# Optimization experiments

Hardware: AMD Instinct MI355X
Metric: run time of the kernel (lower is better)

The kernel has to match this reference:

```python
import jax, jax.numpy as jnp
import numpy as np

B, N_ITEMS, H1, H2 = 1024, 50000, 600, 200


def setup_inputs() -> dict:
    key = jax.random.key(0)
    ks = jax.random.split(key, 8)
    return {
        "x": jax.random.uniform(ks[0], (B, N_ITEMS), dtype=jnp.float32),
        "W1": jax.random.normal(ks[1], (N_ITEMS, H1), dtype=jnp.float32) * 0.02,
        "b1": jax.random.normal(ks[2], (H1,), dtype=jnp.float32) * 0.001,
        "W2": jax.random.normal(ks[3], (H1, H2), dtype=jnp.float32) * 0.05,
        "b2": jax.random.normal(ks[4], (H2,), dtype=jnp.float32) * 0.001,
        "W3": jax.random.normal(ks[5], (H2, H1), dtype=jnp.float32) * 0.05,
        "b3": jax.random.normal(ks[6], (H1,), dtype=jnp.float32) * 0.001,
        "item_emb": jax.random.normal(ks[7], (N_ITEMS, H1), dtype=jnp.float32) * 0.02,
    }


def reference(x, W1, b1, W2, b2, W3, b3, item_emb):
    # F.normalize(input): L2-normalize rows with eps clamp
    norm = jnp.sqrt(jnp.sum(x * x, axis=-1, keepdims=True))
    h = x / jnp.maximum(norm, 1e-12)
    # tanh MLP stack (dropout is identity at inference)
    h = jnp.tanh(h @ W1 + b1)   # [B, 600]
    h = jnp.tanh(h @ W2 + b2)   # [B, 200]
    h = jnp.tanh(h @ W3 + b3)   # [B, 600]
    # pairwise squared-L2 distance to all item embeddings via GEMM decomposition:
    # ||h||^2 - 2 h.e + ||e||^2  (same math as the broadcasted (h-e)^2 sum)
    h_sq = jnp.sum(h * h, axis=-1, keepdims=True)          # [B, 1]
    e_sq = jnp.sum(item_emb * item_emb, axis=-1)           # [N]
    dist = h_sq - 2.0 * (h @ item_emb.T) + e_sq            # [B, N]
    return dist
```

## Files before the change

kernel.cpp:

```cpp
#include <hip/hip_runtime.h>
#include <stdint.h>

namespace {

constexpr int BROWS = 1024;
constexpr int NIT   = 50000;
constexpr int NH1   = 600;
constexpr int NH2   = 200;
constexpr int KXP   = 50048;
constexpr int N1P   = 640;
constexpr int NEP   = 50048;
constexpr int KEP   = 608;
constexpr int KI_TOTAL = KXP / 32;

typedef _Float16 f16x8 __attribute__((ext_vector_type(8)));
typedef _Float16 f16x4 __attribute__((ext_vector_type(4)));
typedef _Float16 f16x2 __attribute__((ext_vector_type(2)));
typedef float    f32x4 __attribute__((ext_vector_type(4)));

__device__ __forceinline__ void gld16(const void* g, void* l) {
  __builtin_amdgcn_global_load_lds(
      (__attribute__((address_space(1))) void*)(void*)g,
      (__attribute__((address_space(3))) void*)l, 16, 0, 0);
}

__global__ __launch_bounds__(256) void norm_conv_k(const float* __restrict__ x,
                                                   float* __restrict__ invnorm,
                                                   _Float16* __restrict__ xh) {
  const int row = blockIdx.x;
  const float4* xr = (const float4*)(x + (size_t)row * NIT);
  float ss = 0.f;
  if (xh != nullptr) {
    f16x4* xo = (f16x4*)(xh + (size_t)row * KXP);
    #pragma unroll 4
    for (int i = threadIdx.x; i < NIT / 4; i += 256) {
      float4 v = xr[i];
      ss += v.x * v.x + v.y * v.y + v.z * v.z + v.w * v.w;
      f16x4 h;
      h.x = (_Float16)v.x; h.y = (_Float16)v.y;
      h.z = (_Float16)v.z; h.w = (_Float16)v.w;
      xo[i] = h;
    }
    if (threadIdx.x < (KXP - NIT) / 4) {
      f16x4 z;
      z.x = (_Float16)0.f; z.y = (_Float16)0.f;
      z.z = (_Float16)0.f; z.w = (_Float16)0.f;
      xo[NIT / 4 + threadIdx.x] = z;
    }
  } else {
    #pragma unroll 4
    for (int i = threadIdx.x; i < NIT / 4; i += 256) {
      float4 v = xr[i];
      ss += v.x * v.x + v.y * v.y + v.z * v.z + v.w * v.w;
    }
  }
  for (int o = 32; o > 0; o >>= 1) ss += __shfl_down(ss, o);
  __shared__ float red[4];
  if ((threadIdx.x & 63) == 0) red[threadIdx.x >> 6] = ss;
  __syncthreads();
  if (threadIdx.x == 0) {
    float s = red[0] + red[1] + red[2] + red[3];
    invnorm[row] = 1.0f / fmaxf(sqrtf(s), 1e-12f);
  }
}

__global__ __launch_bounds__(256) void transpose_w1_k(const float* __restrict__ W1,
                                                      _Float16* __restrict__ W1T) {
  __shared__ float tile[64][65];
  const int kb = blockIdx.x * 64;
  const int nb = blockIdx.y * 64;
  const int t = threadIdx.x;
  #pragma unroll
  for (int i = 0; i < 16; ++i) {
    int idx = i * 256 + t;
    int k = idx >> 6, n = idx & 63;
    int gk = kb + k, gn = nb + n;
    tile[k][n] = (gk < NIT && gn < NH1) ? W1[(size_t)gk * NH1 + gn] : 0.f;
  }
  __syncthreads();
  #pragma unroll
  for (int i = 0; i < 8; ++i) {
    int idx = i * 256 + t;
    int n = idx >> 5;
    int k2 = (idx & 31) * 2;
    f16x2 h;
    h.x = (_Float16)tile[k2][n];
    h.y = (_Float16)tile[k2 + 1][n];
    *(f16x2*)(&W1T[(size_t)(nb + n) * KXP + kb + k2]) = h;
  }
}

__global__ __launch_bounds__(256) void prep_emb_k(const float* __restrict__ emb,
                                                  _Float16* __restrict__ embb,
                                                  float* __restrict__ esq) {
  const int row = blockIdx.x * 4 + (threadIdx.x >> 6);
  const int lane = threadIdx.x & 63;
  const float* er = emb + (size_t)row * NH1;
  float ss = 0.f;
  #pragma unroll
  for (int j = 0; j < 10; ++j) {
    int idx = lane + 64 * j;
    float v = (row < NIT && idx < NH1) ? er[idx] : 0.f;
    ss += v * v;
    if (idx < KEP) embb[(size_t)row * KEP + idx] = (_Float16)v;
  }
  for (int o = 32; o > 0; o >>= 1) ss += __shfl_down(ss, o);
  if (lane == 0) esq[row] = ss;
}

template <int MODE>
__global__ __launch_bounds__(256, 4) void mfma_nt_k(
    const void* __restrict__ Av, const _Float16* __restrict__ Bg,
    float* __restrict__ Cout, const float* __restrict__ hsq,
    const float* __restrict__ esq) {
  __shared__ _Float16 As[2][128 * 32];
  __shared__ _Float16 Bs[2][128 * 32];

  const int t = threadIdx.x;
  const int n0 = blockIdx.x * 128;
  const int m0 = blockIdx.y * 128;

  int ki0, ki1, lda, ldb;
  if (MODE == 1) {
    ki0 = 0; ki1 = KEP / 32; lda = KEP; ldb = KEP;
  } else {
    const int Z = (int)gridDim.z;
    const int kiPer = (KI_TOTAL + Z - 1) / Z;
    ki0 = blockIdx.z * kiPer;
    ki1 = ki0 + kiPer;
    if (ki1 > KI_TOTAL) ki1 = KI_TOTAL;
    lda = (MODE == 0) ? NIT : KXP;
    ldb = KXP;
  }

  const int lane = t & 63;
  const int wid = t >> 6;
  const int wm = wid >> 1, wn = wid & 1;
  const int lrow = lane & 15, quad = lane >> 4;

  const f32x4 zero = {0.f, 0.f, 0.f, 0.f};
  f32x4 acc[4][4];
  #pragma unroll
  for (int i = 0; i < 4; ++i)
    #pragma unroll
    for (int j = 0; j < 4; ++j) acc[i][j] = zero;

  auto stage = [&](int buf, int ki) {
    const int k0 = ki * 32;
    if (MODE == 0) {
      const float* A = (const float*)Av;
      #pragma unroll
      for (int j = 0; j < 4; ++j) {
        int g = j * 256 + t;
        int row = g >> 3;
        int kq = (g & 7) * 4;
        float4 v = {0.f, 0.f, 0.f, 0.f};
        if (k0 + kq < NIT)
          v = *(const float4*)(A + (size_t)(m0 + row) * lda + (k0 + kq));
        f16x4 h;
        h.x = (_Float16)v.x; h.y = (_Float16)v.y;
        h.z = (_Float16)v.z; h.w = (_Float16)v.w;
        *(f16x4*)(&As[buf][row * 32 + kq]) = h;
      }
    } else {
      const _Float16* A = (const _Float16*)Av;
      #pragma unroll
      for (int j = 0; j < 2; ++j) {
        int c = j * 256 + t;
        int row = c >> 2, kk = (c & 3) * 8;
        gld16(A + (size_t)(m0 + row) * lda + (k0 + kk), &As[buf][c * 8]);
      }
    }
    #pragma unroll
    for (int j = 0; j < 2; ++j) {
      int c = j * 256 + t;
      int row = c >> 2, kk = (c & 3) * 8;
      gld16(Bg + (size_t)(n0 + row) * ldb + (k0 + kk), &Bs[buf][c * 8]);
    }
  };

  stage(0, ki0);
  __syncthreads();

  int cur = 0;
  for (int ki = ki0; ki < ki1; ++ki) {
    if (ki + 1 < ki1) stage(cur ^ 1, ki + 1);

    f16x8 af[4], bfr[4];
    #pragma unroll
    for (int mi = 0; mi < 4; ++mi)
      af[mi] = *(const f16x8*)(&As[cur][(wm * 64 + mi * 16 + lrow) * 32 + quad * 8]);
    #pragma unroll
    for (int ni = 0; ni < 4; ++ni)
      bfr[ni] = *(const f16x8*)(&Bs[cur][(wn * 64 + ni * 16 + lrow) * 32 + quad * 8]);
    #pragma unroll
    for (int mi = 0; mi < 4; ++mi)
      #pragma unroll
      for (int ni = 0; ni < 4; ++ni)
        acc[mi][ni] = __builtin_amdgcn_mfma_f32_16x16x32_f16(af[mi], bfr[ni],
                                                             acc[mi][ni], 0, 0, 0);
    __syncthreads();
    cur ^= 1;
  }

  if (MODE != 1) {
    float* Cs = Cout + (size_t)blockIdx.z * BROWS * N1P;
    #pragma unroll
    for (int mi = 0; mi < 4; ++mi)
      #pragma unroll
      for (int r = 0; r < 4; ++r) {
        int row = m0 + wm * 64 + mi * 16 + quad * 4 + r;
        #pragma unroll
        for (int ni = 0; ni < 4; ++ni) {
          int col = n0 + wn * 64 + ni * 16 + lrow;
          Cs[(size_t)row * N1P + col] = acc[mi][ni][r];
        }
      }
  } else {
    #pragma unroll
    for (int mi = 0; mi < 4; ++mi)
      #pragma unroll
      for (int r = 0; r < 4; ++r) {
        int row = m0 + wm * 64 + mi * 16 + quad * 4 + r;
        float hv = hsq[row];
        #pragma unroll
        for (int ni = 0; ni < 4; ++ni) {
          int col = n0 + wn * 64 + ni * 16 + lrow;
          if (col < NIT)
            Cout[(size_t)row * NIT + col] = hv - 2.f * acc[mi][ni][r] + esq[col];
        }
      }
  }
}

__global__ __launch_bounds__(256) void reduce_epi1_k(const float* __restrict__ C1p,
                                                     const float* __restrict__ invnorm,
                                                     const float* __restrict__ b1,
                                                     float* __restrict__ h1,
                                                     int nslabs) {
  int idx = blockIdx.x * 256 + threadIdx.x;
  if (idx >= BROWS * NH1) return;
  int m = idx / NH1, n = idx - m * NH1;
  float s = 0.f;
  for (int sp = 0; sp < nslabs; ++sp)
    s += C1p[(size_t)sp * BROWS * N1P + (size_t)m * N1P + n];
  h1[idx] = tanhf(invnorm[m] * s + b1[n]);
}

__global__ __launch_bounds__(256) void gemm2_k(const float* __restrict__ h1,
                                               const float* __restrict__ W2,
                                               const float* __restrict__ b2,
                                               float* __restrict__ h2) {
  __shared__ float hs[8 * NH1];
  const int m0 = blockIdx.x * 8;
  const int t = threadIdx.x;
  for (int i = t; i < 8 * NH1; i += 256) hs[i] = h1[(size_t)m0 * NH1 + i];
  __syncthreads();
  if (t < NH2) {
    float acc[8];
    #pragma unroll
    for (int r = 0; r < 8; ++r) acc[r] = 0.f;
    for (int k0 = 0; k0 < NH1; k0 += 8) {
      float w[8];
      #pragma unroll
      for (int u = 0; u < 8; ++u) w[u] = W2[(k0 + u) * NH2 + t];
      #pragma unroll
      for (int u = 0; u < 8; ++u)
        #pragma unroll
        for (int r = 0; r < 8; ++r) acc[r] += hs[r * NH1 + k0 + u] * w[u];
    }
    float bb = b2[t];
    #pragma unroll
    for (int r = 0; r < 8; ++r) h2[(size_t)(m0 + r) * NH2 + t] = tanhf(acc[r] + bb);
  }
}

__global__ __launch_bounds__(256) void gemm3_k(const float* __restrict__ h2,
                                               const float* __restrict__ W3,
                                               const float* __restrict__ b3,
                                               _Float16* __restrict__ h3h,
                                               float* __restrict__ hsq) {
  __shared__ float hs[8 * NH2];
  const int m0 = blockIdx.x * 8;
  const int t = threadIdx.x;
  for (int i = t; i < 8 * NH2; i += 256) hs[i] = h2[(size_t)m0 * NH2 + i];
  __syncthreads();
  float ssq[8];
  #pragma unroll
  for (int r = 0; r < 8; ++r) ssq[r] = 0.f;
  for (int c = 0; c < 3; ++c) {
    int n = t + c * 256;
    if (n < NH1) {
      float acc[8];
      #pragma unroll
      for (int r = 0; r < 8; ++r) acc[r] = 0.f;
      for (int k0 = 0; k0 < NH2; k0 += 8) {
        float w[8];
        #pragma unroll
        for (int u = 0; u < 8; ++u) w[u] = W3[(k0 + u) * NH1 + n];
        #pragma unroll
        for (int u = 0; u < 8; ++u)
          #pragma unroll
          for (int r = 0; r < 8; ++r) acc[r] += hs[r * NH2 + k0 + u] * w[u];
      }
      float bb = b3[n];
      #pragma unroll
      for (int r = 0; r < 8; ++r) {
        float v = tanhf(acc[r] + bb);
        h3h[(size_t)(m0 + r) * KEP + n] = (_Float16)v;
        ssq[r] += v * v;
      }
    } else if (n < KEP) {
      #pragma unroll
      for (int r = 0; r < 8; ++r) h3h[(size_t)(m0 + r) * KEP + n] = (_Float16)0.f;
    }
  }
  const int lane = t & 63, wid = t >> 6;
  #pragma unroll
  for (int r = 0; r < 8; ++r)
    for (int o = 32; o > 0; o >>= 1) ssq[r] += __shfl_down(ssq[r], o);
  __shared__ float red2[8][4];
  if (lane == 0) {
    #pragma unroll
    for (int r = 0; r < 8; ++r) red2[r][wid] = ssq[r];
  }
  __syncthreads();
  if (t < 8) hsq[m0 + t] = red2[t][0] + red2[t][1] + red2[t][2] + red2[t][3];
}

}

extern "C" void kernel_launch(void* const* d_in, const int* in_sizes, int n_in,
                              void* d_out, int out_size, void* d_ws, size_t ws_size,
                              hipStream_t stream) {
  const float* x   = (const float*)d_in[0];
  const float* W1  = (const float*)d_in[1];
  const float* b1  = (const float*)d_in[2];
  const float* W2  = (const float*)d_in[3];
  const float* b2  = (const float*)d_in[4];
  const float* W3  = (const float*)d_in[5];
  const float* b3  = (const float*)d_in[6];
  const float* emb = (const float*)d_in[7];
  float* out = (float*)d_out;

  char* ws = (char*)d_ws;

  const size_t XHSZ  = (size_t)BROWS * KXP * 2;
  const size_t W1TSZ = (size_t)N1P * KXP * 2;
  const size_t SLAB  = (size_t)BROWS * N1P * 4;
  const size_t TAIL  = 4096 + 200192 + 2457600 + 819200 + 1245184 + 4096;

  bool useF16A;
  int S;
  const size_t baseA = XHSZ + W1TSZ + TAIL;
  const size_t baseB = W1TSZ + TAIL;
  if (ws_size >= baseA + 16 * SLAB) {
    useF16A = true;
    size_t s = (ws_size - baseA) / SLAB;
    S = s > 32 ? 32 : (int)s;
  } else if (ws_size >= baseB + 8 * SLAB) {
    useF16A = false;
    size_t s = (ws_size - baseB) / SLAB;
    S = s > 32 ? 32 : (int)s;
  } else {
    return;
  }

  size_t off = 0;
  _Float16* xh = nullptr;
  if (useF16A) { xh = (_Float16*)(ws + off); off += XHSZ; }
  const size_t oW1T = off;
  _Float16* W1T = (_Float16*)(ws + off); off += W1TSZ;
  float* C1p = (float*)(ws + off); off += (size_t)S * SLAB;
  float* invn = (float*)(ws + off); off += 4096;
  float* esq  = (float*)(ws + off); off += 200192;
  float* h1   = (float*)(ws + off); off += 2457600;
  float* h2   = (float*)(ws + off); off += 819200;
  _Float16* h3h = (_Float16*)(ws + off); off += 1245184;
  float* hsq  = (float*)(ws + off); off += 4096;
  _Float16* embb = (_Float16*)(ws + oW1T);

  norm_conv_k<<<dim3(BROWS), dim3(256), 0, stream>>>(x, invn, xh);
  transpose_w1_k<<<dim3(KXP / 64, N1P / 64), dim3(256), 0, stream>>>(W1, W1T);
  if (useF16A) {
    mfma_nt_k<2><<<dim3(N1P / 128, BROWS / 128, S), dim3(256), 0, stream>>>(
        (const void*)xh, W1T, C1p, nullptr, nullptr);
  } else {
    mfma_nt_k<0><<<dim3(N1P / 128, BROWS / 128, S), dim3(256), 0, stream>>>(
        (const void*)x, W1T, C1p, nullptr, nullptr);
  }
  reduce_epi1_k<<<dim3((BROWS * NH1 + 255) / 256), dim3(256), 0, stream>>>(
      C1p, invn, b1, h1, S);
  prep_emb_k<<<dim3(NEP / 4), dim3(256), 0, stream>>>(emb, embb, esq);
  gemm2_k<<<dim3(BROWS / 8), dim3(256), 0, stream>>>(h1, W2, b2, h2);
  gemm3_k<<<dim3(BROWS / 8), dim3(256), 0, stream>>>(h2, W3, b3, h3h, hsq);
  mfma_nt_k<1><<<dim3(NEP / 128, BROWS / 128, 1), dim3(256), 0, stream>>>(
      (const void*)h3h, embb, out, hsq, esq);
}
```

Baseline: 1.010 ms.

## Use BK=64 single-buffered swizzled LDS tiles and XCD-aware block remapping in MFMA GEMMs

The MFMA GEMM kernel now uses 64-wide K tiles with an XOR-swizzled LDS layout, replacing the 32-wide double-buffered tiles, which halves the number of barrier iterations and aims to avoid LDS bank conflicts. Workgroup IDs are remapped so that consecutive blocks landing on the same XCD share A/B tiles in L2. The embedding K padding grows to 640 to fit the 64-wide step. Dropping double buffering loses the overlap between global loads and compute within a block, so latency hiding now depends on occupancy.

```diff
diff --git a/kernel.cpp b/kernel.cpp
--- a/kernel.cpp
+++ b/kernel.cpp
@@ -10,8 +10,10 @@
 constexpr int KXP   = 50048;
 constexpr int N1P   = 640;
 constexpr int NEP   = 50048;
-constexpr int KEP   = 608;
-constexpr int KI_TOTAL = KXP / 32;
+constexpr int KEP   = 640;
+constexpr int KI64_TOTAL = KXP / 64;
+constexpr int NBLK1 = N1P / 128;
+constexpr int NBLK4 = NEP / 128;
 
 typedef _Float16 f16x8 __attribute__((ext_vector_type(8)));
 typedef _Float16 f16x4 __attribute__((ext_vector_type(4)));
@@ -102,7 +104,7 @@
     int idx = lane + 64 * j;
     float v = (row < NIT && idx < NH1) ? er[idx] : 0.f;
     ss += v * v;
-    if (idx < KEP) embb[(size_t)row * KEP + idx] = (_Float16)v;
+    embb[(size_t)row * KEP + idx] = (_Float16)v;
   }
   for (int o = 32; o > 0; o >>= 1) ss += __shfl_down(ss, o);
   if (lane == 0) esq[row] = ss;
@@ -113,22 +115,31 @@
     const void* __restrict__ Av, const _Float16* __restrict__ Bg,
     float* __restrict__ Cout, const float* __restrict__ hsq,
     const float* __restrict__ esq) {
-  __shared__ _Float16 As[2][128 * 32];
-  __shared__ _Float16 Bs[2][128 * 32];
+  __shared__ _Float16 As[128 * 64];
+  __shared__ _Float16 Bs[128 * 64];
 
   const int t = threadIdx.x;
-  const int n0 = blockIdx.x * 128;
-  const int m0 = blockIdx.y * 128;
-
-  int ki0, ki1, lda, ldb;
+
+  int n0, m0, ki0, ki1, zslab = 0, lda, ldb;
   if (MODE == 1) {
-    ki0 = 0; ki1 = KEP / 32; lda = KEP; ldb = KEP;
+    int flat = blockIdx.x + NBLK4 * blockIdx.y;
+    int W = (flat & 7) * (NBLK4 * 8 / 8) + (flat >> 3);
+    m0 = (W & 7) * 128;
+    n0 = (W >> 3) * 128;
+    ki0 = 0; ki1 = KEP / 64;
+    lda = KEP; ldb = KEP;
   } else {
-    const int Z = (int)gridDim.z;
-    const int kiPer = (KI_TOTAL + Z - 1) / Z;
-    ki0 = blockIdx.z * kiPer;
-    ki1 = ki0 + kiPer;
-    if (ki1 > KI_TOTAL) ki1 = KI_TOTAL;
+    const int S = (int)gridDim.z;
+    int flat = blockIdx.x + NBLK1 * (blockIdx.y + 8 * blockIdx.z);
+    int W = (flat & 7) * (5 * S) + (flat >> 3);
+    int xq = W % 5;
+    int yz = W / 5;
+    n0 = xq * 128;
+    m0 = (yz & 7) * 128;
+    zslab = yz >> 3;
+    int kiPer = (KI64_TOTAL + S - 1) / S;
+    ki0 = zslab * kiPer;
+    ki1 = ki0 + kiPer; if (ki1 > KI64_TOTAL) ki1 = KI64_TOTAL;
     lda = (MODE == 0) ? NIT : KXP;
     ldb = KXP;
   }
@@ -145,66 +156,71 @@
     #pragma unroll
     for (int j = 0; j < 4; ++j) acc[i][j] = zero;
 
-  auto stage = [&](int buf, int ki) {
-    const int k0 = ki * 32;
+  for (int ki = ki0; ki < ki1; ++ki) {
+    const int k0 = ki * 64;
     if (MODE == 0) {
       const float* A = (const float*)Av;
       #pragma unroll
-      for (int j = 0; j < 4; ++j) {
+      for (int j = 0; j < 8; ++j) {
         int g = j * 256 + t;
-        int row = g >> 3;
-        int kq = (g & 7) * 4;
+        int row = g >> 4;
+        int q4 = g & 15;
+        int kcol = k0 + q4 * 4;
         float4 v = {0.f, 0.f, 0.f, 0.f};
-        if (k0 + kq < NIT)
-          v = *(const float4*)(A + (size_t)(m0 + row) * lda + (k0 + kq));
+        if (kcol < NIT)
+          v = *(const float4*)(A + (size_t)(m0 + row) * lda + kcol);
         f16x4 h;
         h.x = (_Float16)v.x; h.y = (_Float16)v.y;
         h.z = (_Float16)v.z; h.w = (_Float16)v.w;
-        *(f16x4*)(&As[buf][row * 32 + kq]) = h;
+        int c16 = (q4 >> 1) ^ (row & 7);
+        *(f16x4*)(&As[row * 64 + c16 * 8 + (q4 & 1) * 4]) = h;
       }
     } else {
       const _Float16* A = (const _Float16*)Av;
       #pragma unroll
-      for (int j = 0; j < 2; ++j) {
+      for (int j = 0; j < 4; ++j) {
         int c = j * 256 + t;
-        int row = c >> 2, kk = (c & 3) * 8;
-        gld16(A + (size_t)(m0 + row) * lda + (k0 + kk), &As[buf][c * 8]);
-      }
-    }
-    #pragma unroll
-    for (int j = 0; j < 2; ++j) {
+        int row = c >> 3;
+        int kk = ((c & 7) ^ (row & 7)) << 3;
+        gld16(A + (size_t)(m0 + row) * lda + (k0 + kk), &As[c * 8]);
+      }
+    }
+    #pragma unroll
+    for (int j = 0; j < 4; ++j) {
       int c = j * 256 + t;
-      int row = c >> 2, kk = (c & 3) * 8;
-      gld16(Bg + (size_t)(n0 + row) * ldb + (k0 + kk), &Bs[buf][c * 8]);
-    }
-  };
-
-  stage(0, ki0);
-  __syncthreads();
-
-  int cur = 0;
-  for (int ki = ki0; ki < ki1; ++ki) {
-    if (ki + 1 < ki1) stage(cur ^ 1, ki + 1);
-
-    f16x8 af[4], bfr[4];
-    #pragma unroll
-    for (int mi = 0; mi < 4; ++mi)
-      af[mi] = *(const f16x8*)(&As[cur][(wm * 64 + mi * 16 + lrow) * 32 + quad * 8]);
-    #pragma unroll
-    for (int ni = 0; ni < 4; ++ni)
-      bfr[ni] = *(const f16x8*)(&Bs[cur][(wn * 64 + ni * 16 + lrow) * 32 + quad * 8]);
-    #pragma unroll
-    for (int mi = 0; mi < 4; ++mi)
-      #pragma unroll
-      for (int ni = 0; ni < 4; ++ni)
-        acc[mi][ni] = __builtin_amdgcn_mfma_f32_16x16x32_f16(af[mi], bfr[ni],
-                                                             acc[mi][ni], 0, 0, 0);
+      int row = c >> 3;
+      int kk = ((c & 7) ^ (row & 7)) << 3;
+      gld16(Bg + (size_t)(n0 + row) * ldb + (k0 + kk), &Bs[c * 8]);
+    }
     __syncthreads();
-    cur ^= 1;
+
+    #pragma unroll
+    for (int ks = 0; ks < 2; ++ks) {
+      f16x8 af[4], bfr[4];
+      #pragma unroll
+      for (int mi = 0; mi < 4; ++mi) {
+        int row = wm * 64 + mi * 16 + lrow;
+        int c16 = (ks * 4 + quad) ^ (lrow & 7);
+        af[mi] = *(const f16x8*)(&As[row * 64 + c16 * 8]);
+      }
+      #pragma unroll
+      for (int ni = 0; ni < 4; ++ni) {
+        int row = wn * 64 + ni * 16 + lrow;
+        int c16 = (ks * 4 + quad) ^ (lrow & 7);
+        bfr[ni] = *(const f16x8*)(&Bs[row * 64 + c16 * 8]);
+      }
+      #pragma unroll
+      for (int mi = 0; mi < 4; ++mi)
+        #pragma unroll
+        for (int ni = 0; ni < 4; ++ni)
+          acc[mi][ni] = __builtin_amdgcn_mfma_f32_16x16x32_f16(af[mi], bfr[ni],
+                                                               acc[mi][ni], 0, 0, 0);
+    }
+    __syncthreads();
   }
 
   if (MODE != 1) {
-    float* Cs = Cout + (size_t)blockIdx.z * BROWS * N1P;
+    float* Cs = Cout + (size_t)zslab * BROWS * N1P;
     #pragma unroll
     for (int mi = 0; mi < 4; ++mi)
       #pragma unroll
@@ -348,7 +364,7 @@
   const size_t XHSZ  = (size_t)BROWS * KXP * 2;
   const size_t W1TSZ = (size_t)N1P * KXP * 2;
   const size_t SLAB  = (size_t)BROWS * N1P * 4;
-  const size_t TAIL  = 4096 + 200192 + 2457600 + 819200 + 1245184 + 4096;
+  const size_t TAIL  = 4096 + 200192 + 2457600 + 819200 + 1310720 + 4096;
 
   bool useF16A;
   int S;
@@ -376,17 +392,17 @@
   float* esq  = (float*)(ws + off); off += 200192;
   float* h1   = (float*)(ws + off); off += 2457600;
   float* h2   = (float*)(ws + off); off += 819200;
-  _Float16* h3h = (_Float16*)(ws + off); off += 1245184;
+  _Float16* h3h = (_Float16*)(ws + off); off += 1310720;
   float* hsq  = (float*)(ws + off); off += 4096;
   _Float16* embb = (_Float16*)(ws + oW1T);
 
   norm_conv_k<<<dim3(BROWS), dim3(256), 0, stream>>>(x, invn, xh);
   transpose_w1_k<<<dim3(KXP / 64, N1P / 64), dim3(256), 0, stream>>>(W1, W1T);
   if (useF16A) {
-    mfma_nt_k<2><<<dim3(N1P / 128, BROWS / 128, S), dim3(256), 0, stream>>>(
+    mfma_nt_k<2><<<dim3(NBLK1, BROWS / 128, S), dim3(256), 0, stream>>>(
         (const void*)xh, W1T, C1p, nullptr, nullptr);
   } else {
-    mfma_nt_k<0><<<dim3(N1P / 128, BROWS / 128, S), dim3(256), 0, stream>>>(
+    mfma_nt_k<0><<<dim3(NBLK1, BROWS / 128, S), dim3(256), 0, stream>>>(
         (const void*)x, W1T, C1p, nullptr, nullptr);
   }
   reduce_epi1_k<<<dim3((BROWS * NH1 + 255) / 256), dim3(256), 0, stream>>>(
@@ -394,6 +410,6 @@
   prep_emb_k<<<dim3(NEP / 4), dim3(256), 0, stream>>>(emb, embb, esq);
   gemm2_k<<<dim3(BROWS / 8), dim3(256), 0, stream>>>(h1, W2, b2, h2);
   gemm3_k<<<dim3(BROWS / 8), dim3(256), 0, stream>>>(h2, W3, b3, h3h, hsq);
-  mfma_nt_k<1><<<dim3(NEP / 128, BROWS / 128, 1), dim3(256), 0, stream>>>(
+  mfma_nt_k<1><<<dim3(NBLK4, BROWS / 128, 1), dim3(256), 0, stream>>>(
       (const void*)h3h, embb, out, hsq, esq);
 }
```

Result: faster. 863.5 us (-14.5%).
